# Kernel tuning notes

Hardware: AMD Instinct MI355X
Metric: run time of the kernel (lower is better)

Reference implementation:

```python
import jax, jax.numpy as jnp
import numpy as np
import math

B, N0 = 128, 128          # graphs, nodes per graph
EPG = 512                 # edges per graph
F_IN, EDGE_DIM = 64, 16
EMB, HEADS = 128, 4
HC = EMB * HEADS
L = 2                     # stacked layers (pooling every layer: top_k_every_n=1)
RATIO = 0.5
DENSE = 256


def setup_inputs():
    rng = np.random.default_rng(0)

    def U(fan_in, *shape):
        s = 1.0 / np.sqrt(fan_in)
        return jnp.asarray(rng.uniform(-s, s, shape), dtype=jnp.float32)

    x = jnp.asarray(rng.standard_normal((B * N0, F_IN)), dtype=jnp.float32)
    src = rng.integers(0, N0, (B, EPG))
    dst = rng.integers(0, N0, (B, EPG))
    off = (np.arange(B) * N0)[:, None]
    edge_index = jnp.asarray(np.stack([(src + off).reshape(-1), (dst + off).reshape(-1)]), dtype=jnp.int32)
    edge_attr = jnp.asarray(rng.standard_normal((B * EPG, EDGE_DIM)), dtype=jnp.float32)

    inp = dict(x=x, edge_index=edge_index, edge_attr=edge_attr)
    inp.update(
        c1_Wq=U(F_IN, F_IN, HC), c1_bq=U(F_IN, HC),
        c1_Wk=U(F_IN, F_IN, HC), c1_bk=U(F_IN, HC),
        c1_Wv=U(F_IN, F_IN, HC), c1_bv=U(F_IN, HC),
        c1_We=U(EDGE_DIM, EDGE_DIM, HC),
        c1_Ws=U(F_IN, F_IN, HC), c1_bs=U(F_IN, HC),
        c1_Wb=U(3 * HC, 3 * HC),
        t1_W=U(HC, HC, EMB), t1_b=U(HC, EMB),
        bn1_g=jnp.ones(EMB), bn1_b=jnp.zeros(EMB),
        cl_Wq=U(EMB, L, EMB, HC), cl_bq=U(EMB, L, HC),
        cl_Wk=U(EMB, L, EMB, HC), cl_bk=U(EMB, L, HC),
        cl_Wv=U(EMB, L, EMB, HC), cl_bv=U(EMB, L, HC),
        cl_We=U(EDGE_DIM, L, EDGE_DIM, HC),
        cl_Ws=U(EMB, L, EMB, HC), cl_bs=U(EMB, L, HC),
        cl_Wb=U(3 * HC, L, 3 * HC),
        tl_W=U(HC, L, HC, EMB), tl_b=U(HC, L, EMB),
        bnl_g=jnp.ones((L, EMB)), bnl_b=jnp.zeros((L, EMB)),
        pool_w=U(EMB, L, EMB),
        l1_W=U(2 * EMB, 2 * EMB, DENSE), l1_b=U(2 * EMB, DENSE),
        l2_W=U(DENSE, DENSE, DENSE // 2), l2_b=U(DENSE, DENSE // 2),
        l3_W=U(DENSE // 2, DENSE // 2, 1), l3_b=U(DENSE // 2, 1),
    )
    return inp


def _tconv(x, src, dst, emask, ea, Wq, bq, Wk, bk, Wv, bv, We, Ws, bs, Wb, n_nodes):
    # PyG TransformerConv, beta=True, concat=True, edge features added to key and value
    H, C = HEADS, EMB
    q = (x @ Wq + bq).reshape(-1, H, C)
    k = (x @ Wk + bk).reshape(-1, H, C)
    v = (x @ Wv + bv).reshape(-1, H, C)
    e = (ea @ We).reshape(-1, H, C)
    kj = k[src] + e
    alpha = (q[dst] * kj).sum(-1) * (1.0 / math.sqrt(C))  # [E, H]
    mx = jax.ops.segment_max(jnp.where(emask[:, None], alpha, -jnp.inf), dst, num_segments=n_nodes)
    mx = jnp.where(jnp.isfinite(mx), mx, 0.0)
    p = jnp.where(emask[:, None], jnp.exp(alpha - mx[dst]), 0.0)
    p = p / (jax.ops.segment_sum(p, dst, num_segments=n_nodes)[dst] + 1e-16)
    msg = v[src] + e
    out = jax.ops.segment_sum(p[:, :, None] * msg, dst, num_segments=n_nodes).reshape(-1, H * C)
    skip = x @ Ws + bs
    beta = jax.nn.sigmoid(jnp.concatenate([out, skip, out - skip], -1) @ Wb)[:, None]
    return beta * skip + (1.0 - beta) * out


def _bn(x, g, b):
    # BatchNorm1d, training-mode batch statistics (biased variance)
    m = x.mean(0)
    v = ((x - m) ** 2).mean(0)
    return g * (x - m) * jax.lax.rsqrt(v + 1e-5) + b


def _topk_pool(x, src, dst, emask, w, n):
    # TopKPooling: score = x.w/|w|, keep top ceil(ratio*n) per graph, scale by tanh(score)
    k = int(math.ceil(RATIO * n))
    s = (x @ w) / jnp.linalg.norm(w)          # [B*n]
    _, idx = jax.lax.top_k(s.reshape(B, n), k)
    idx = jnp.sort(idx, axis=1)
    gidx = (jnp.arange(B)[:, None] * n + idx).reshape(-1)
    x_new = x[gidx] * jnp.tanh(s[gidx])[:, None]
    kept = jnp.zeros(B * n, bool).at[gidx].set(True)
    new_id = (jnp.cumsum(kept) - 1).astype(jnp.int32)
    em = emask & kept[src] & kept[dst]
    src_n = jnp.where(em, new_id[src], 0)
    dst_n = jnp.where(em, new_id[dst], 0)
    return x_new, src_n, dst_n, em, k


def _forward(edge_index, x, edge_attr, c1_Wq, c1_bq, c1_Wk, c1_bk, c1_Wv, c1_bv, c1_We, c1_Ws, c1_bs, c1_Wb,
             t1_W, t1_b, bn1_g, bn1_b, cl_Wq, cl_bq, cl_Wk, cl_bk, cl_Wv, cl_bv, cl_We, cl_Ws, cl_bs, cl_Wb,
             tl_W, tl_b, bnl_g, bnl_b, pool_w, l1_W, l1_b, l2_W, l2_b, l3_W, l3_b):
    src, dst = edge_index[0], edge_index[1]
    emask = jnp.ones(src.shape[0], bool)
    n = N0
    x = _tconv(x, src, dst, emask, edge_attr, c1_Wq, c1_bq, c1_Wk, c1_bk, c1_Wv, c1_bv, c1_We, c1_Ws, c1_bs, c1_Wb, B * n)
    x = _bn(jax.nn.relu(x @ t1_W + t1_b), bn1_g, bn1_b)
    reps = []
    for i in range(L):
        x = _tconv(x, src, dst, emask, edge_attr, cl_Wq[i], cl_bq[i], cl_Wk[i], cl_bk[i], cl_Wv[i], cl_bv[i],
                   cl_We[i], cl_Ws[i], cl_bs[i], cl_Wb[i], B * n)
        x = _bn(jax.nn.relu(x @ tl_W[i] + tl_b[i]), bnl_g[i], bnl_b[i])
        x, src, dst, emask, n = _topk_pool(x, src, dst, emask, pool_w[i], n)
        xg = x.reshape(B, n, EMB)
        reps.append(jnp.concatenate([xg.max(1), xg.mean(1)], -1))  # gmp || gap
    h = reps[0]
    for r in reps[1:]:
        h = h + r
    h = jax.nn.relu(h @ l1_W + l1_b)  # dropout p=0.8 is identity at eval
    h = jax.nn.relu(h @ l2_W + l2_b)
    return h @ l3_W + l3_b            # [B, 1]


def reference(x, edge_index, edge_attr, c1_Wq, c1_bq, c1_Wk, c1_bk, c1_Wv, c1_bv, c1_We, c1_Ws, c1_bs, c1_Wb,
              t1_W, t1_b, bn1_g, bn1_b, cl_Wq, cl_bq, cl_Wk, cl_bk, cl_Wv, cl_bv, cl_We, cl_Ws, cl_bs, cl_Wb,
              tl_W, tl_b, bnl_g, bnl_b, pool_w, l1_W, l1_b, l2_W, l2_b, l3_W, l3_b):
    return _forward(edge_index, x, edge_attr, c1_Wq, c1_bq, c1_Wk, c1_bk, c1_Wv, c1_bv, c1_We, c1_Ws, c1_bs, c1_Wb,
                    t1_W, t1_b, bn1_g, bn1_b, cl_Wq, cl_bq, cl_Wk, cl_bk, cl_Wv, cl_bv, cl_We, cl_Ws, cl_bs, cl_Wb,
                    tl_W, tl_b, bnl_g, bnl_b, pool_w, l1_W, l1_b, l2_W, l2_b, l3_W, l3_b)
```

## Files before the change

### kernel.cpp

```cpp
#include <hip/hip_runtime.h>
#include <math.h>

#define E_TOT 65536
#define B_G   128
#define QLD   1664
#define NCOL  1792

typedef __attribute__((ext_vector_type(8))) short short8;
typedef __attribute__((ext_vector_type(4))) short short4v;
typedef __attribute__((ext_vector_type(4))) float float4v;

__device__ __forceinline__ unsigned short f2bf(float f) {
    unsigned int u = __float_as_uint(f);
    unsigned int r = u + 0x7FFFu + ((u >> 16) & 1u);
    return (unsigned short)(r >> 16);
}
__device__ __forceinline__ float bf2f(unsigned short h) {
    return __uint_as_float(((unsigned int)h) << 16);
}

struct LayerPrep {
    const float *Ws, *bs_, *Wq, *bq, *We, *Wv, *bv, *tW;
    float *Wst, *ws_z, *sbt, *zb, *Wu, *bu, *Wet, *wez, *Wvt, *bvt, *Wvz, *bvz;
    unsigned short *Whi, *Wlo;
    int Fin;
};

__device__ __forceinline__ LayerPrep pick(const LayerPrep& p0, const LayerPrep& p1,
                                          const LayerPrep& p2) {
    return blockIdx.y == 0 ? p0 : (blockIdx.y == 1 ? p1 : p2);
}

__global__ void prep_all_k(LayerPrep p0, LayerPrep p1, LayerPrep p2, const float* Wb0,
                           const float* Wb1, const float* Wb2) {
    LayerPrep p = pick(p0, p1, p2);
    const float* Wb = blockIdx.y == 0 ? Wb0 : (blockIdx.y == 1 ? Wb1 : Wb2);
    int Fin = p.Fin;
    int w = blockIdx.x * 4 + (threadIdx.x >> 6);
    int lane = threadIdx.x & 63;

    int U1 = Fin * 2;
    int U2 = U1 + 2;
    int U3 = U2 + Fin * 8;
    int U4 = U3 + 8;
    int U5 = U4 + 128;
    if (w < U5) {
        const float* A; const float* bp; float* outp; int R;
        if (w < U1) {
            int f = w >> 1, m0 = (w & 1) * 64;
            A = p.Ws + (size_t)f * 512; bp = p.tW + m0 + lane;
            outp = p.Wst + f * 128 + m0 + lane; R = 512;
        } else if (w < U2) {
            int m0 = (w - U1) * 64;
            A = p.bs_; bp = p.tW + m0 + lane;
            outp = p.sbt + m0 + lane; R = 512;
        } else if (w < U3) {
            int u = w - U2; int f = u >> 3, q = u & 7;
            int cb = (q >> 1) * 128, m0 = (q & 1) * 64;
            A = p.Wv + (size_t)f * 512 + cb; bp = p.tW + cb * 128 + m0 + lane;
            outp = p.Wvt + (size_t)f * 512 + q * 64 + lane; R = 128;
        } else if (w < U4) {
            int q = w - U3; int cb = (q >> 1) * 128, m0 = (q & 1) * 64;
            A = p.bv + cb; bp = p.tW + cb * 128 + m0 + lane;
            outp = p.bvt + q * 64 + lane; R = 128;
        } else {
            int u = w - U4; int j2 = u >> 1, m0 = (u & 1) * 64;
            int j = j2 & 15, cb = (j2 >> 4) * 128;
            A = p.We + j * 512 + cb; bp = p.tW + cb * 128 + m0 + lane;
            outp = p.Wet + j2 * 128 + m0 + lane; R = 128;
        }
        float a0 = 0.f, a1 = 0.f, a2 = 0.f, a3 = 0.f;
        for (int c = 0; c < R; c += 4) {
            a0 = fmaf(A[c],     bp[0],   a0);
            a1 = fmaf(A[c + 1], bp[128], a1);
            a2 = fmaf(A[c + 2], bp[256], a2);
            a3 = fmaf(A[c + 3], bp[384], a3);
            bp += 512;
        }
        *outp = (a0 + a1) + (a2 + a3);
        return;
    }

    int w2 = w - U5;
    int q1 = Fin, q2 = q1 + 1, q3 = q2 + Fin * 64, q4 = q3 + 64, q5 = q4 + 64;
    int q6 = q5 + Fin * 4, q7 = q6 + 4;
    if (w2 >= q7) return;
    float s = 0.f;
    if (w2 < q1) {
        int f = w2;
        for (int c = lane; c < 512; c += 64)
            s = fmaf(p.Ws[(size_t)f * 512 + c], Wb[512 + c] - Wb[1024 + c], s);
    } else if (w2 < q2) {
        for (int c = lane; c < 512; c += 64)
            s = fmaf(p.bs_[c], Wb[512 + c] - Wb[1024 + c], s);
    } else if (w2 < q3) {
        int q = w2 - q2; int f = q >> 6; int j2 = q & 63;
        int j = j2 & 15; int cb = (j2 >> 4) * 128;
        s = p.Wq[(size_t)f * 512 + cb + lane] * p.We[j * 512 + cb + lane]
          + p.Wq[(size_t)f * 512 + cb + lane + 64] * p.We[j * 512 + cb + lane + 64];
    } else if (w2 < q4) {
        int j2 = w2 - q3; int j = j2 & 15; int cb = (j2 >> 4) * 128;
        s = p.bq[cb + lane] * p.We[j * 512 + cb + lane]
          + p.bq[cb + lane + 64] * p.We[j * 512 + cb + lane + 64];
    } else if (w2 < q5) {
        int j2 = w2 - q4; int j = j2 & 15; int cb = (j2 >> 4) * 128;
        s = p.We[j * 512 + cb + lane] * (Wb[cb + lane] + Wb[1024 + cb + lane])
          + p.We[j * 512 + cb + lane + 64] * (Wb[cb + lane + 64] + Wb[1024 + cb + lane + 64]);
    } else if (w2 < q6) {
        int q = w2 - q5; int f = q >> 2; int cb = (q & 3) * 128;
        s = p.Wv[(size_t)f * 512 + cb + lane] * (Wb[cb + lane] + Wb[1024 + cb + lane])
          + p.Wv[(size_t)f * 512 + cb + lane + 64] * (Wb[cb + lane + 64] + Wb[1024 + cb + lane + 64]);
    } else {
        int cb = (w2 - q6) * 128;
        s = p.bv[cb + lane] * (Wb[cb + lane] + Wb[1024 + cb + lane])
          + p.bv[cb + lane + 64] * (Wb[cb + lane + 64] + Wb[1024 + cb + lane + 64]);
    }
#pragma unroll
    for (int off = 32; off; off >>= 1) s += __shfl_xor(s, off, 64);
    if (lane == 0) {
        if (w2 < q1) p.ws_z[w2] = s;
        else if (w2 < q2) p.zb[0] = s;
        else if (w2 < q3) p.Wu[w2 - q2] = s;
        else if (w2 < q4) p.bu[w2 - q3] = s;
        else if (w2 < q5) p.wez[w2 - q4] = s;
        else if (w2 < q6) p.Wvz[w2 - q5] = s;
        else p.bvz[w2 - q6] = s;
    }
}

__global__ void wsplit_all_k(LayerPrep p0, LayerPrep p1, LayerPrep p2,
                             const float* Wk0, const float* Wk1, const float* Wk2) {
    LayerPrep p = pick(p0, p1, p2);
    const float* Wk = blockIdx.y == 0 ? Wk0 : (blockIdx.y == 1 ? Wk1 : Wk2);
    int K = p.Fin, kshift = (K == 64) ? 6 : 7;
    int idx = blockIdx.x * 256 + threadIdx.x;
    if (idx >= NCOL * K) return;
    int col = idx >> kshift, k = idx & (K - 1);
    float w;
    if (col < 128)       w = p.Wst[k * 128 + col];
    else if (col < 640)  w = p.Wq[(size_t)k * 512 + col - 128];
    else if (col < 1152) w = Wk[(size_t)k * 512 + col - 640];
    else if (col < 1664) w = p.Wvt[(size_t)k * 512 + col - 1152];
    else if (col < 1728) w = p.Wu[(size_t)k * 64 + col - 1664];
    else if (col < 1732) w = p.Wvz[(size_t)k * 4 + col - 1728];
    else if (col == 1732) w = p.ws_z[k];
    else                 w = 0.f;
    unsigned short h = f2bf(w);
    p.Whi[idx] = h;
    p.Wlo[idx] = f2bf(w - bf2f(h));
}

__global__ void xsplit_k(const float* __restrict__ X, int total4,
                         unsigned short* __restrict__ Xhi, unsigned short* __restrict__ Xlo) {
    int idx = blockIdx.x * 256 + threadIdx.x;
    if (idx >= total4) return;
    float4 f = ((const float4*)X)[idx];
    unsigned short h0 = f2bf(f.x), h1 = f2bf(f.y), h2 = f2bf(f.z), h3 = f2bf(f.w);
    short4v hv = {(short)h0, (short)h1, (short)h2, (short)h3};
    short4v lv = {(short)f2bf(f.x - bf2f(h0)), (short)f2bf(f.y - bf2f(h1)),
                  (short)f2bf(f.z - bf2f(h2)), (short)f2bf(f.w - bf2f(h3))};
    *(short4v*)(Xhi + (size_t)idx * 4) = hv;
    *(short4v*)(Xlo + (size_t)idx * 4) = lv;
}

template <int KT>
__global__ __launch_bounds__(256) void qkvs_mfma(
        const unsigned short* __restrict__ Xhi, const unsigned short* __restrict__ Xlo,
        const unsigned short* __restrict__ Whi, const unsigned short* __restrict__ Wlo,
        const float* __restrict__ bq, const float* __restrict__ bk,
        const float* __restrict__ bvt, const float* __restrict__ bu,
        const float* __restrict__ bvz, const float* __restrict__ zb,
        float* __restrict__ out, float* __restrict__ UB, float* __restrict__ VZB,
        float* __restrict__ SZB, int nwg8) {
    constexpr int NKC = KT >> 5;
    constexpr int NCH = KT >> 6;
    __shared__ __align__(16) unsigned short bs[NCH * 2 * 64 * 80];
    const int ldb = 80;
    int tid = threadIdx.x;
    int wave = tid >> 6, lane = tid & 63;
    int m = lane & 15, kg = lane >> 4;
    int hw = blockIdx.y * 28 + blockIdx.x;
    int lb = (hw & 7) * nwg8 + (hw >> 3);
    int rb = (lb / 28) * 256;
    int c0 = (lb % 28) * 64;

    short8 ahi[2][NKC], alo[2][NKC];
    auto loadA = [&](int n0) {
#pragma unroll
        for (int rt = 0; rt < 2; ++rt) {
            const unsigned short* xh = Xhi + (size_t)(n0 + rt * 16 + m) * KT + kg * 8;
            const unsigned short* xl = Xlo + (size_t)(n0 + rt * 16 + m) * KT + kg * 8;
#pragma unroll
            for (int kc = 0; kc < NKC; ++kc) {
                ahi[rt][kc] = *(const short8*)(xh + kc * 32);
                alo[rt][kc] = *(const short8*)(xl + kc * 32);
            }
        }
    };
    loadA(rb + wave * 32);

    for (int i = tid; i < NCH * 64 * 8; i += 256) {
        int ch = i >> 9;
        int r = i & 511; int col = r >> 3, part = r & 7;
        unsigned short* dst = bs + ch * (2 * 64 * 80);
        *(short8*)(dst + col * ldb + part * 8) =
            *(const short8*)(Whi + (size_t)(c0 + col) * KT + ch * 64 + part * 8);
        *(short8*)(dst + 64 * 80 + col * ldb + part * 8) =
            *(const short8*)(Wlo + (size_t)(c0 + col) * KT + ch * 64 + part * 8);
    }
    __syncthreads();

    float bias[4];
#pragma unroll
    for (int ct = 0; ct < 4; ++ct) {
        int col = c0 + ct * 16 + m;
        float bv_;
        if (col < 128)       bv_ = 0.f;
        else if (col < 640)  bv_ = bq[col - 128];
        else if (col < 1152) bv_ = bk[col - 640];
        else if (col < 1664) bv_ = bvt[col - 1152];
        else if (col < 1728) bv_ = bu[col - 1664];
        else if (col < 1732) bv_ = bvz[col - 1728];
        else if (col == 1732) bv_ = zb[0];
        else                 bv_ = 0.f;
        bias[ct] = bv_;
    }

#pragma unroll
    for (int rg = 0; rg < 2; ++rg) {
        int n0 = rb + rg * 128 + wave * 32;
        if (rg) loadA(n0);

        float4v acc[2][4];
#pragma unroll
        for (int rt = 0; rt < 2; ++rt)
#pragma unroll
            for (int ct = 0; ct < 4; ++ct) acc[rt][ct] = (float4v){0.f, 0.f, 0.f, 0.f};

#pragma unroll
        for (int ch = 0; ch < NCH; ++ch) {
            const unsigned short* bsc = bs + ch * (2 * 64 * 80);
#pragma unroll
            for (int kc2 = 0; kc2 < 2; ++kc2) {
                const int kc = ch * 2 + kc2;
#pragma unroll
                for (int ct = 0; ct < 4; ++ct) {
                    const unsigned short* bp = bsc + (ct * 16 + m) * ldb + kg * 8 + kc2 * 32;
                    short8 bhi = *(const short8*)(bp);
                    short8 blo = *(const short8*)(bp + 64 * 80);
                    acc[0][ct] = __builtin_amdgcn_mfma_f32_16x16x32_bf16(ahi[0][kc], bhi, acc[0][ct], 0, 0, 0);
                    acc[0][ct] = __builtin_amdgcn_mfma_f32_16x16x32_bf16(alo[0][kc], bhi, acc[0][ct], 0, 0, 0);
                    acc[0][ct] = __builtin_amdgcn_mfma_f32_16x16x32_bf16(ahi[0][kc], blo, acc[0][ct], 0, 0, 0);
                    acc[1][ct] = __builtin_amdgcn_mfma_f32_16x16x32_bf16(ahi[1][kc], bhi, acc[1][ct], 0, 0, 0);
                    acc[1][ct] = __builtin_amdgcn_mfma_f32_16x16x32_bf16(alo[1][kc], bhi, acc[1][ct], 0, 0, 0);
                    acc[1][ct] = __builtin_amdgcn_mfma_f32_16x16x32_bf16(ahi[1][kc], blo, acc[1][ct], 0, 0, 0);
                }
            }
        }

#pragma unroll
        for (int ct = 0; ct < 4; ++ct) {
            int col = c0 + ct * 16 + m;
            if (col > 1732) continue;
#pragma unroll
            for (int rt = 0; rt < 2; ++rt) {
#pragma unroll
                for (int r = 0; r < 4; ++r) {
                    int row = n0 + rt * 16 + kg * 4 + r;
                    float v = acc[rt][ct][r] + bias[ct];
                    if (col < 1664)      out[(size_t)row * QLD + col] = v;
                    else if (col < 1728) UB[(size_t)row * 64 + col - 1664] = v;
                    else if (col < 1732) VZB[(size_t)row * 4 + col - 1728] = v;
                    else                 SZB[row] = v;
                }
            }
        }
    }
}

__global__ __launch_bounds__(128) void csr_graph_k(const int* __restrict__ src,
                                                   const int* __restrict__ dst,
                                                   int* __restrict__ row_start,
                                                   int* __restrict__ row_end,
                                                   int* __restrict__ colb,
                                                   int* __restrict__ eidb) {
    __shared__ int cnt[128], pref[128], cur[128];
    int g = blockIdx.x, t = threadIdx.x;
    cnt[t] = 0;
    __syncthreads();
    int e0 = g * 512, nb = g * 128;
    int dl[4], sl[4];
#pragma unroll
    for (int i = 0; i < 4; ++i) {
        int e = e0 + t + i * 128;
        dl[i] = dst[e] - nb;
        sl[i] = src[e];
        atomicAdd(&cnt[dl[i]], 1);
    }
    __syncthreads();
    pref[t] = cnt[t];
    __syncthreads();
    for (int st = 1; st < 128; st <<= 1) {
        int v = (t >= st) ? pref[t - st] : 0;
        __syncthreads();
        pref[t] += v;
        __syncthreads();
    }
    int ex = pref[t] - cnt[t];
    row_start[nb + t] = e0 + ex;
    row_end[nb + t]   = e0 + pref[t];
    cur[t] = ex;
    __syncthreads();
#pragma unroll
    for (int i = 0; i < 4; ++i) {
        int pos = atomicAdd(&cur[dl[i]], 1);
        colb[e0 + pos] = sl[i];
        eidb[e0 + pos] = e0 + t + i * 128;
    }
}

__global__ __launch_bounds__(256) void attn_combine_k(
        const float* __restrict__ QB, const float* __restrict__ UB,
        const float* __restrict__ VZB, const float* __restrict__ SZB,
        const int* __restrict__ row_start, const int* __restrict__ row_end,
        const int* __restrict__ colb, const int* __restrict__ eidb,
        const float* __restrict__ ea, const float* __restrict__ wez,
        const float* __restrict__ Wet, const float* __restrict__ sbt,
        const float* __restrict__ tb, float* __restrict__ xn, int nwg8) {
    __shared__ float shO[4][4][128];
    __shared__ float tsh[4][64];
    __shared__ float zsh[4][4];
    int tid = threadIdx.x;
    int head = tid >> 6, lane = tid & 63;
    int grp = lane >> 4, li = lane & 15;
    int bid = blockIdx.x;
    int lb = (bid & 7) * nwg8 + (bid >> 3);
    int node = lb * 4 + grp;

    float wezv = wez[head * 16 + li];
    const float* Qr = QB + (size_t)node * QLD + 128 + head * 128 + li * 8;
    float4 q0 = *(const float4*)Qr;
    float4 q1 = *(const float4*)(Qr + 4);
    float uu = UB[(size_t)node * 64 + head * 16 + li];
    int beg = row_start[node], end = row_end[node];

    float l = 0.f, t = 0.f, zac = 0.f;
    float4 a0 = {0.f, 0.f, 0.f, 0.f}, a1 = {0.f, 0.f, 0.f, 0.f};
    const float scale = 0.08838834764831845f;
    int j = beg;
    for (; j + 1 < end; j += 2) {
        int s1 = colb[j],     e1 = eidb[j];
        int s2 = colb[j + 1], e2 = eidb[j + 1];
        const float* K1 = QB + (size_t)s1 * QLD + 640 + head * 128 + li * 8;
        const float* V1 = QB + (size_t)s1 * QLD + 1152 + head * 128 + li * 8;
        const float* K2 = QB + (size_t)s2 * QLD + 640 + head * 128 + li * 8;
        const float* V2 = QB + (size_t)s2 * QLD + 1152 + head * 128 + li * 8;
        float4 k10 = *(const float4*)K1, k11 = *(const float4*)(K1 + 4);
        float4 v10 = *(const float4*)V1, v11 = *(const float4*)(V1 + 4);
        float4 k20 = *(const float4*)K2, k21 = *(const float4*)(K2 + 4);
        float4 v20 = *(const float4*)V2, v21 = *(const float4*)(V2 + 4);
        float ea1 = ea[(size_t)e1 * 16 + li];
        float ea2 = ea[(size_t)e2 * 16 + li];
        float vz1 = VZB[(size_t)s1 * 4 + head];
        float vz2 = VZB[(size_t)s2 * 4 + head];
        float p1 = q0.x * k10.x + q0.y * k10.y + q0.z * k10.z + q0.w * k10.w
                 + q1.x * k11.x + q1.y * k11.y + q1.z * k11.z + q1.w * k11.w + ea1 * uu;
        float p2 = q0.x * k20.x + q0.y * k20.y + q0.z * k20.z + q0.w * k20.w
                 + q1.x * k21.x + q1.y * k21.y + q1.z * k21.z + q1.w * k21.w + ea2 * uu;
        p1 += __shfl_xor(p1, 1, 64); p1 += __shfl_xor(p1, 2, 64);
        p1 += __shfl_xor(p1, 4, 64); p1 += __shfl_xor(p1, 8, 64);
        p2 += __shfl_xor(p2, 1, 64); p2 += __shfl_xor(p2, 2, 64);
        p2 += __shfl_xor(p2, 4, 64); p2 += __shfl_xor(p2, 8, 64);
        float w1 = expf(p1 * scale), w2 = expf(p2 * scale);
        l += w1; l += w2;
        t = fmaf(w1, ea1, t); t = fmaf(w2, ea2, t);
        zac = fmaf(w1, vz1, zac); zac = fmaf(w2, vz2, zac);
        a0.x = fmaf(w1, v10.x, a0.x); a0.y = fmaf(w1, v10.y, a0.y);
        a0.z = fmaf(w1, v10.z, a0.z); a0.w = fmaf(w1, v10.w, a0.w);
        a1.x = fmaf(w1, v11.x, a1.x); a1.y = fmaf(w1, v11.y, a1.y);
        a1.z = fmaf(w1, v11.z, a1.z); a1.w = fmaf(w1, v11.w, a1.w);
        a0.x = fmaf(w2, v20.x, a0.x); a0.y = fmaf(w2, v20.y, a0.y);
        a0.z = fmaf(w2, v20.z, a0.z); a0.w = fmaf(w2, v20.w, a0.w);
        a1.x = fmaf(w2, v21.x, a1.x); a1.y = fmaf(w2, v21.y, a1.y);
        a1.z = fmaf(w2, v21.z, a1.z); a1.w = fmaf(w2, v21.w, a1.w);
    }
    if (j < end) {
        int s1 = colb[j], e1 = eidb[j];
        const float* K1 = QB + (size_t)s1 * QLD + 640 + head * 128 + li * 8;
        const float* V1 = QB + (size_t)s1 * QLD + 1152 + head * 128 + li * 8;
        float4 k10 = *(const float4*)K1, k11 = *(const float4*)(K1 + 4);
        float4 v10 = *(const float4*)V1, v11 = *(const float4*)(V1 + 4);
        float ea1 = ea[(size_t)e1 * 16 + li];
        float vz1 = VZB[(size_t)s1 * 4 + head];
        float p1 = q0.x * k10.x + q0.y * k10.y + q0.z * k10.z + q0.w * k10.w
                 + q1.x * k11.x + q1.y * k11.y + q1.z * k11.z + q1.w * k11.w + ea1 * uu;
        p1 += __shfl_xor(p1, 1, 64); p1 += __shfl_xor(p1, 2, 64);
        p1 += __shfl_xor(p1, 4, 64); p1 += __shfl_xor(p1, 8, 64);
        float w1 = expf(p1 * scale);
        l += w1;
        t = fmaf(w1, ea1, t);
        zac = fmaf(w1, vz1, zac);
        a0.x = fmaf(w1, v10.x, a0.x); a0.y = fmaf(w1, v10.y, a0.y);
        a0.z = fmaf(w1, v10.z, a0.z); a0.w = fmaf(w1, v10.w, a0.w);
        a1.x = fmaf(w1, v11.x, a1.x); a1.y = fmaf(w1, v11.y, a1.y);
        a1.z = fmaf(w1, v11.z, a1.z); a1.w = fmaf(w1, v11.w, a1.w);
    }

    float inv = 1.f / (l + 1e-16f);
    float tn = t * inv;
    float zw = tn * wezv;
    zw += __shfl_xor(zw, 1, 64); zw += __shfl_xor(zw, 2, 64);
    zw += __shfl_xor(zw, 4, 64); zw += __shfl_xor(zw, 8, 64);
    float z = zac * inv + zw;

    float* op = &shO[grp][head][li * 8];
    op[0] = a0.x * inv; op[1] = a0.y * inv; op[2] = a0.z * inv; op[3] = a0.w * inv;
    op[4] = a1.x * inv; op[5] = a1.y * inv; op[6] = a1.z * inv; op[7] = a1.w * inv;
    tsh[grp][head * 16 + li] = tn;
    if (li == 0) zsh[grp][head] = z;
    __syncthreads();

    int dim = tid & 127;
    int nsBase = tid >> 7;
    float sb = sbt[dim], tbv = tb[dim];
    float wet0 = 0.f, wet1 = 0.f;
#pragma unroll 8
    for (int jj = 0; jj < 64; ++jj) {
        float wv = Wet[jj * 128 + dim];
        wet0 = fmaf(tsh[nsBase][jj], wv, wet0);
        wet1 = fmaf(tsh[nsBase + 2][jj], wv, wet1);
    }
#pragma unroll
    for (int r = 0; r < 2; ++r) {
        int ns = nsBase + r * 2;
        float wet = r ? wet1 : wet0;
        int nd = lb * 4 + ns;
        float outT = shO[ns][0][dim] + shO[ns][1][dim] + shO[ns][2][dim] + shO[ns][3][dim] + wet;
        float zt = zsh[ns][0] + zsh[ns][1] + zsh[ns][2] + zsh[ns][3] + SZB[nd];
        float beta = 1.f / (1.f + expf(-zt));
        float S = QB[(size_t)nd * QLD + dim];
        float a = beta * (S + sb) + (1.f - beta) * outT + tbv;
        xn[(size_t)nd * 128 + dim] = fmaxf(a, 0.f);
    }
}

__global__ void bn_stats_k(const float* __restrict__ x, int N, float* __restrict__ stats) {
    int c = threadIdx.x;
    float s = 0.f, ss = 0.f;
    for (int n = blockIdx.x; n < N; n += gridDim.x) {
        float v = x[(size_t)n * 128 + c];
        s += v; ss += v * v;
    }
    atomicAdd(&stats[c], s);
    atomicAdd(&stats[128 + c], ss);
}

__global__ void bn_apply_k(float* __restrict__ x, int N, const float* __restrict__ stats,
                           const float* __restrict__ g, const float* __restrict__ b,
                           unsigned short* __restrict__ Xhi, unsigned short* __restrict__ Xlo) {
    int idx = blockIdx.x * blockDim.x + threadIdx.x;
    if (idx >= N * 128) return;
    int c = idx & 127;
    float m = stats[c] / (float)N;
    float var = fmaxf(stats[128 + c] / (float)N - m * m, 0.f);
    float inv = rsqrtf(var + 1e-5f);
    float v = g[c] * (x[idx] - m) * inv + b[c];
    x[idx] = v;
    unsigned short h = f2bf(v);
    Xhi[idx] = h;
    Xlo[idx] = f2bf(v - bf2f(h));
}

__global__ void bn_apply_score_k(float* __restrict__ x, int N, const float* __restrict__ stats,
                                 const float* __restrict__ g, const float* __restrict__ b,
                                 const float* __restrict__ w, float* __restrict__ s) {
    int node = blockIdx.x * 4 + (threadIdx.x >> 6);
    int lane = threadIdx.x & 63;
    int c0 = lane, c1 = lane + 64;
    float m0 = stats[c0] / (float)N;
    float v0 = fmaxf(stats[128 + c0] / (float)N - m0 * m0, 0.f);
    float m1 = stats[c1] / (float)N;
    float v1 = fmaxf(stats[128 + c1] / (float)N - m1 * m1, 0.f);
    float* row = x + (size_t)node * 128;
    float x0 = g[c0] * (row[c0] - m0) * rsqrtf(v0 + 1e-5f) + b[c0];
    float x1 = g[c1] * (row[c1] - m1) * rsqrtf(v1 + 1e-5f) + b[c1];
    row[c0] = x0;
    row[c1] = x1;
    float w0 = w[c0], w1 = w[c1];
    float p  = x0 * w0 + x1 * w1;
    float nw = w0 * w0 + w1 * w1;
#pragma unroll
    for (int off = 32; off; off >>= 1) {
        p  += __shfl_xor(p, off, 64);
        nw += __shfl_xor(nw, off, 64);
    }
    if (lane == 0) s[node] = p / sqrtf(nw);
}

__global__ __launch_bounds__(128) void topk_pool0_k(
        const float* __restrict__ sc, const float* __restrict__ x,
        const int* __restrict__ src, const int* __restrict__ dst,
        float* __restrict__ xp, float* __restrict__ rep,
        int* __restrict__ row_start, int* __restrict__ row_end,
        int* __restrict__ colb, int* __restrict__ eidb,
        unsigned short* __restrict__ Xhi, unsigned short* __restrict__ Xlo) {
    __shared__ float ls[128], th[64];
    __shared__ int lk[128], rk[128], oon[64];
    __shared__ int cnt[64], pref[64], cur[64];
    int g = blockIdx.x, t = threadIdx.x;
    float val = sc[g * 128 + t];
    ls[t] = val;
    __syncthreads();
    int c = 0;
    for (int j = 0; j < 128; ++j) {
        float vj = ls[j];
        c += (vj > val || (vj == val && j < t)) ? 1 : 0;
    }
    int kp = (c < 64) ? 1 : 0;
    lk[t] = kp;
    __syncthreads();
    int r = 0;
    for (int j = 0; j < t; ++j) r += lk[j];
    rk[t] = r;
    if (kp) { oon[r] = t; th[r] = tanhf(val); }
    __syncthreads();
    float mx = -INFINITY, sm = 0.f;
    for (int rr = 0; rr < 64; ++rr) {
        float v = x[(size_t)(g * 128 + oon[rr]) * 128 + t] * th[rr];
        int oidx = (g * 64 + rr) * 128 + t;
        xp[oidx] = v;
        unsigned short h = f2bf(v);
        Xhi[oidx] = h;
        Xlo[oidx] = f2bf(v - bf2f(h));
        mx = fmaxf(mx, v);
        sm += v;
    }
    rep[g * 256 + t] = mx;
    rep[g * 256 + 128 + t] = sm * (1.f / 64.f);
    if (t < 64) cnt[t] = 0;
    __syncthreads();
    int e0 = g * 512, nb = g * 128;
    int keepE[4], dr[4], sr[4];
#pragma unroll
    for (int i = 0; i < 4; ++i) {
        int e = e0 + t + i * 128;
        int s_ = src[e] - nb, d_ = dst[e] - nb;
        int ke = lk[s_] && lk[d_];
        keepE[i] = ke;
        dr[i] = rk[d_];
        sr[i] = rk[s_];
        if (ke) atomicAdd(&cnt[dr[i]], 1);
    }
    __syncthreads();
    if (t < 64) pref[t] = cnt[t];
    __syncthreads();
    for (int st = 1; st < 64; st <<= 1) {
        int v = (t < 64 && t >= st) ? pref[t - st] : 0;
        __syncthreads();
        if (t < 64) pref[t] += v;
        __syncthreads();
    }
    if (t < 64) {
        int ex = pref[t] - cnt[t];
        row_start[g * 64 + t] = e0 + ex;
        row_end[g * 64 + t]   = e0 + pref[t];
        cur[t] = ex;
    }
    __syncthreads();
#pragma unroll
    for (int i = 0; i < 4; ++i) {
        if (keepE[i]) {
            int pos = atomicAdd(&cur[dr[i]], 1);
            colb[e0 + pos] = g * 64 + sr[i];
            eidb[e0 + pos] = e0 + t + i * 128;
        }
    }
}

__global__ __launch_bounds__(128) void topk_pool1_k(
        const float* __restrict__ sc, const float* __restrict__ x,
        float* __restrict__ rep) {
    __shared__ float ls[64], th[32];
    __shared__ int lk[64], oon[32];
    int g = blockIdx.x, t = threadIdx.x;
    float val = 0.f;
    if (t < 64) { val = sc[g * 64 + t]; ls[t] = val; }
    __syncthreads();
    if (t < 64) {
        int c = 0;
        for (int j = 0; j < 64; ++j) {
            float vj = ls[j];
            c += (vj > val || (vj == val && j < t)) ? 1 : 0;
        }
        int kp = (c < 32) ? 1 : 0;
        lk[t] = kp;
    }
    __syncthreads();
    if (t < 64 && lk[t]) {
        int r = 0;
        for (int j = 0; j < t; ++j) r += lk[j];
        oon[r] = t;
        th[r] = tanhf(val);
    }
    __syncthreads();
    float mx = -INFINITY, sm = 0.f;
    for (int rr = 0; rr < 32; ++rr) {
        float v = x[(size_t)(g * 64 + oon[rr]) * 128 + t] * th[rr];
        mx = fmaxf(mx, v);
        sm += v;
    }
    rep[g * 256 + t] = mx;
    rep[g * 256 + 128 + t] = sm * (1.f / 32.f);
}

__global__ void head_k(const float* __restrict__ rep0, const float* __restrict__ rep1,
                       const float* __restrict__ W1, const float* __restrict__ b1,
                       const float* __restrict__ W2, const float* __restrict__ b2,
                       const float* __restrict__ W3, const float* __restrict__ b3,
                       float* __restrict__ out) {
    __shared__ float h[256], a1[256], a2[128], red[256];
    int g = blockIdx.x, t = threadIdx.x;
    h[t] = rep0[g * 256 + t] + rep1[g * 256 + t];
    __syncthreads();
    float acc = b1[t];
    for (int i = 0; i < 256; ++i) acc = fmaf(h[i], W1[i * 256 + t], acc);
    a1[t] = fmaxf(acc, 0.f);
    __syncthreads();
    if (t < 128) {
        float a = b2[t];
        for (int i = 0; i < 256; ++i) a = fmaf(a1[i], W2[i * 128 + t], a);
        a2[t] = fmaxf(a, 0.f);
    }
    __syncthreads();
    red[t] = (t < 128) ? a2[t] * W3[t] : 0.f;
    __syncthreads();
    for (int st = 128; st; st >>= 1) {
        if (t < st) red[t] += red[t + st];
        __syncthreads();
    }
    if (t == 0) out[g] = red[0] + b3[0];
}

extern "C" void kernel_launch(void* const* d_in, const int* in_sizes, int n_in,
                              void* d_out, int out_size, void* d_ws, size_t ws_size,
                              hipStream_t stream) {
    (void)in_sizes; (void)n_in; (void)out_size; (void)ws_size;

    const float* x0    = (const float*)d_in[0];
    const int*   ei    = (const int*)d_in[1];
    const float* ea    = (const float*)d_in[2];
    const float* c1_Wq = (const float*)d_in[3];
    const float* c1_bq = (const float*)d_in[4];
    const float* c1_Wk = (const float*)d_in[5];
    const float* c1_bk = (const float*)d_in[6];
    const float* c1_Wv = (const float*)d_in[7];
    const float* c1_bv = (const float*)d_in[8];
    const float* c1_We = (const float*)d_in[9];
    const float* c1_Ws = (const float*)d_in[10];
    const float* c1_bs = (const float*)d_in[11];
    const float* c1_Wb = (const float*)d_in[12];
    const float* t1_W  = (const float*)d_in[13];
    const float* t1_b  = (const float*)d_in[14];
    const float* bn1_g = (const float*)d_in[15];
    const float* bn1_b = (const float*)d_in[16];
    const float* cl_Wq = (const float*)d_in[17];
    const float* cl_bq = (const float*)d_in[18];
    const float* cl_Wk = (const float*)d_in[19];
    const float* cl_bk = (const float*)d_in[20];
    const float* cl_Wv = (const float*)d_in[21];
    const float* cl_bv = (const float*)d_in[22];
    const float* cl_We = (const float*)d_in[23];
    const float* cl_Ws = (const float*)d_in[24];
    const float* cl_bs = (const float*)d_in[25];
    const float* cl_Wb = (const float*)d_in[26];
    const float* tl_W  = (const float*)d_in[27];
    const float* tl_b  = (const float*)d_in[28];
    const float* bnl_g = (const float*)d_in[29];
    const float* bnl_b = (const float*)d_in[30];
    const float* pool_w= (const float*)d_in[31];
    const float* l1_W  = (const float*)d_in[32];
    const float* l1_b  = (const float*)d_in[33];
    const float* l2_W  = (const float*)d_in[34];
    const float* l2_b  = (const float*)d_in[35];
    const float* l3_W  = (const float*)d_in[36];
    const float* l3_b  = (const float*)d_in[37];
    float* out = (float*)d_out;

    char* base = (char*)d_ws;
    size_t off = 0;
    auto alloc = [&](size_t bytes) -> void* {
        void* p = base + off;
        off += (bytes + 255) & ~(size_t)255;
        return p;
    };
    float* QB   = (float*)alloc((size_t)16384 * QLD * 4);
    float* xA   = (float*)alloc((size_t)16384 * 128 * 4);
    float* xB   = (float*)alloc((size_t)16384 * 128 * 4);
    float* UB   = (float*)alloc((size_t)16384 * 64 * 4);
    float* VZB  = (float*)alloc((size_t)16384 * 4 * 4);
    float* SZB  = (float*)alloc((size_t)16384 * 4);
    float* stats  = (float*)alloc(256 * 4);
    float* scores = (float*)alloc(16384 * 4);
    float* rep0   = (float*)alloc(128 * 256 * 4);
    float* rep1   = (float*)alloc(128 * 256 * 4);
    int* row_start = (int*)alloc(16384 * 4);
    int* row_end   = (int*)alloc(16384 * 4);
    int* colb      = (int*)alloc(E_TOT * 4);
    int* eidb      = (int*)alloc(E_TOT * 4);
    unsigned short* Xhi = (unsigned short*)alloc((size_t)16384 * 128 * 2);
    unsigned short* Xlo = (unsigned short*)alloc((size_t)16384 * 128 * 2);

    LayerPrep P[3];
    const float* Wb_[3] = {c1_Wb, cl_Wb, cl_Wb + 1536};
    const float* Wk_[3] = {c1_Wk, cl_Wk, cl_Wk + 65536};
    for (int l = 0; l < 3; ++l) {
        LayerPrep& p = P[l];
        p.Wst  = (float*)alloc(128 * 128 * 4);
        p.ws_z = (float*)alloc(128 * 4);
        p.sbt  = (float*)alloc(128 * 4);
        p.zb   = (float*)alloc(16);
        p.Wu   = (float*)alloc(128 * 64 * 4);
        p.bu   = (float*)alloc(64 * 4);
        p.Wet  = (float*)alloc(64 * 128 * 4);
        p.wez  = (float*)alloc(64 * 4);
        p.Wvt  = (float*)alloc(128 * 512 * 4);
        p.bvt  = (float*)alloc(512 * 4);
        p.Wvz  = (float*)alloc(128 * 4 * 4);
        p.bvz  = (float*)alloc(16);
        p.Whi  = (unsigned short*)alloc((size_t)NCOL * 128 * 2);
        p.Wlo  = (unsigned short*)alloc((size_t)NCOL * 128 * 2);
    }
    P[0].Ws = c1_Ws; P[0].bs_ = c1_bs; P[0].Wq = c1_Wq; P[0].bq = c1_bq;
    P[0].We = c1_We; P[0].Wv = c1_Wv; P[0].bv = c1_bv; P[0].tW = t1_W; P[0].Fin = 64;
    P[1].Ws = cl_Ws; P[1].bs_ = cl_bs; P[1].Wq = cl_Wq; P[1].bq = cl_bq;
    P[1].We = cl_We; P[1].Wv = cl_Wv; P[1].bv = cl_bv; P[1].tW = tl_W; P[1].Fin = 128;
    P[2].Ws = cl_Ws + 65536; P[2].bs_ = cl_bs + 512; P[2].Wq = cl_Wq + 65536;
    P[2].bq = cl_bq + 512; P[2].We = cl_We + 8192; P[2].Wv = cl_Wv + 65536;
    P[2].bv = cl_bv + 512; P[2].tW = tl_W + 65536; P[2].Fin = 128;

    float* xp = xA;

    {
        int unitsMax = (10 * 128 + 138) + (69 * 128 + 133);
        prep_all_k<<<dim3((unitsMax + 3) / 4, 3), 256, 0, stream>>>(P[0], P[1], P[2],
                                                                    Wb_[0], Wb_[1], Wb_[2]);
        wsplit_all_k<<<dim3((NCOL * 128 + 255) / 256, 3), 256, 0, stream>>>(P[0], P[1], P[2],
                                                                            Wk_[0], Wk_[1], Wk_[2]);
    }

    csr_graph_k<<<B_G, 128, 0, stream>>>(ei, ei + E_TOT, row_start, row_end, colb, eidb);
    xsplit_k<<<(16384 * 64 / 4 + 255) / 256, 256, 0, stream>>>(x0, 16384 * 64 / 4, Xhi, Xlo);

    auto tconv = [&](int L, int N, const float* bq, const float* bk, const float* tb,
                     float* xn) {
        int nwg8 = 28 * (N / 256) / 8;
        if (P[L].Fin == 64)
            qkvs_mfma<64><<<dim3(28, N / 256), 256, 0, stream>>>(Xhi, Xlo, P[L].Whi, P[L].Wlo,
                                                                 bq, bk, P[L].bvt, P[L].bu,
                                                                 P[L].bvz, P[L].zb,
                                                                 QB, UB, VZB, SZB, nwg8);
        else
            qkvs_mfma<128><<<dim3(28, N / 256), 256, 0, stream>>>(Xhi, Xlo, P[L].Whi, P[L].Wlo,
                                                                  bq, bk, P[L].bvt, P[L].bu,
                                                                  P[L].bvz, P[L].zb,
                                                                  QB, UB, VZB, SZB, nwg8);
        attn_combine_k<<<N / 4, 256, 0, stream>>>(QB, UB, VZB, SZB,
                                                  row_start, row_end, colb, eidb,
                                                  ea, P[L].wez, P[L].Wet, P[L].sbt, tb,
                                                  xn, N / 32);
    };

    tconv(0, 16384, c1_bq, c1_bk, t1_b, xA);
    hipMemsetAsync(stats, 0, 256 * 4, stream);
    bn_stats_k<<<512, 128, 0, stream>>>(xA, 16384, stats);
    bn_apply_k<<<(16384 * 128 + 255) / 256, 256, 0, stream>>>(xA, 16384, stats, bn1_g, bn1_b,
                                                              Xhi, Xlo);

    tconv(1, 16384, cl_bq, cl_bk, tl_b, xB);
    hipMemsetAsync(stats, 0, 256 * 4, stream);
    bn_stats_k<<<512, 128, 0, stream>>>(xB, 16384, stats);
    bn_apply_score_k<<<16384 / 4, 256, 0, stream>>>(xB, 16384, stats, bnl_g, bnl_b,
                                                    pool_w, scores);

    topk_pool0_k<<<B_G, 128, 0, stream>>>(scores, xB, ei, ei + E_TOT, xp, rep0,
                                          row_start, row_end, colb, eidb, Xhi, Xlo);

    tconv(2, 8192, cl_bq + 512, cl_bk + 512, tl_b + 128, xB);
    hipMemsetAsync(stats, 0, 256 * 4, stream);
    bn_stats_k<<<512, 128, 0, stream>>>(xB, 8192, stats);
    bn_apply_score_k<<<8192 / 4, 256, 0, stream>>>(xB, 8192, stats, bnl_g + 128, bnl_b + 128,
                                                   pool_w + 128, scores);

    topk_pool1_k<<<B_G, 128, 0, stream>>>(scores, xB, rep1);

    head_k<<<B_G, 256, 0, stream>>>(rep0, rep1, l1_W, l1_b, l2_W, l2_b, l3_W, l3_b, out);
}
```

Measured before the change: 521.8 us.

## Halve qkvs GEMM row tile and stream weight chunks through register double-buffer

The QKV/skip GEMM kernel now handles 128 rows per workgroup instead of 256, which doubles the grid and removes the second row-group pass. Weight tiles are no longer staged into LDS all at once. Each 64-wide K chunk is prefetched into registers one step ahead and written into a single-chunk LDS buffer, which cuts LDS use and overlaps global loads with MFMA work. The cost is that weight tiles are loaded from global memory twice as often across the grid, and there is an extra barrier per chunk.

```diff
diff --git a/kernel.cpp b/kernel.cpp
--- a/kernel.cpp
+++ b/kernel.cpp
@@ -174,105 +174,102 @@
         float* __restrict__ SZB, int nwg8) {
     constexpr int NKC = KT >> 5;
     constexpr int NCH = KT >> 6;
-    __shared__ __align__(16) unsigned short bs[NCH * 2 * 64 * 80];
-    const int ldb = 80;
+    __shared__ __align__(16) unsigned short bs[2 * 64 * 80];
+    const int ldb = 80, loHalf = 64 * 80;
     int tid = threadIdx.x;
     int wave = tid >> 6, lane = tid & 63;
     int m = lane & 15, kg = lane >> 4;
     int hw = blockIdx.y * 28 + blockIdx.x;
     int lb = (hw & 7) * nwg8 + (hw >> 3);
-    int rb = (lb / 28) * 256;
+    int n0 = (lb / 28) * 128 + wave * 32;
     int c0 = (lb % 28) * 64;
 
     short8 ahi[2][NKC], alo[2][NKC];
-    auto loadA = [&](int n0) {
-#pragma unroll
-        for (int rt = 0; rt < 2; ++rt) {
-            const unsigned short* xh = Xhi + (size_t)(n0 + rt * 16 + m) * KT + kg * 8;
-            const unsigned short* xl = Xlo + (size_t)(n0 + rt * 16 + m) * KT + kg * 8;
-#pragma unroll
-            for (int kc = 0; kc < NKC; ++kc) {
-                ahi[rt][kc] = *(const short8*)(xh + kc * 32);
-                alo[rt][kc] = *(const short8*)(xl + kc * 32);
+#pragma unroll
+    for (int rt = 0; rt < 2; ++rt) {
+        const unsigned short* xh = Xhi + (size_t)(n0 + rt * 16 + m) * KT + kg * 8;
+        const unsigned short* xl = Xlo + (size_t)(n0 + rt * 16 + m) * KT + kg * 8;
+#pragma unroll
+        for (int kc = 0; kc < NKC; ++kc) {
+            ahi[rt][kc] = *(const short8*)(xh + kc * 32);
+            alo[rt][kc] = *(const short8*)(xl + kc * 32);
+        }
+    }
+
+    float4v acc[2][4];
+#pragma unroll
+    for (int rt = 0; rt < 2; ++rt)
+#pragma unroll
+        for (int ct = 0; ct < 4; ++ct) acc[rt][ct] = (float4v){0.f, 0.f, 0.f, 0.f};
+
+    short8 ph[2][2], pl[2][2];
+#pragma unroll
+    for (int it = 0; it < 2; ++it) {
+        int i = tid + it * 256; int col = i >> 3, part = i & 7;
+        ph[0][it] = *(const short8*)(Whi + (size_t)(c0 + col) * KT + part * 8);
+        pl[0][it] = *(const short8*)(Wlo + (size_t)(c0 + col) * KT + part * 8);
+    }
+
+#pragma unroll
+    for (int ch = 0; ch < NCH; ++ch) {
+        if (ch) __syncthreads();
+#pragma unroll
+        for (int it = 0; it < 2; ++it) {
+            int i = tid + it * 256; int col = i >> 3, part = i & 7;
+            *(short8*)(bs + col * ldb + part * 8) = ph[ch & 1][it];
+            *(short8*)(bs + loHalf + col * ldb + part * 8) = pl[ch & 1][it];
+        }
+        __syncthreads();
+        if (ch + 1 < NCH) {
+#pragma unroll
+            for (int it = 0; it < 2; ++it) {
+                int i = tid + it * 256; int col = i >> 3, part = i & 7;
+                ph[(ch + 1) & 1][it] =
+                    *(const short8*)(Whi + (size_t)(c0 + col) * KT + (ch + 1) * 64 + part * 8);
+                pl[(ch + 1) & 1][it] =
+                    *(const short8*)(Wlo + (size_t)(c0 + col) * KT + (ch + 1) * 64 + part * 8);
             }
         }
-    };
-    loadA(rb + wave * 32);
-
-    for (int i = tid; i < NCH * 64 * 8; i += 256) {
-        int ch = i >> 9;
-        int r = i & 511; int col = r >> 3, part = r & 7;
-        unsigned short* dst = bs + ch * (2 * 64 * 80);
-        *(short8*)(dst + col * ldb + part * 8) =
-            *(const short8*)(Whi + (size_t)(c0 + col) * KT + ch * 64 + part * 8);
-        *(short8*)(dst + 64 * 80 + col * ldb + part * 8) =
-            *(const short8*)(Wlo + (size_t)(c0 + col) * KT + ch * 64 + part * 8);
-    }
-    __syncthreads();
-
-    float bias[4];
+#pragma unroll
+        for (int kc2 = 0; kc2 < 2; ++kc2) {
+            const int kc = ch * 2 + kc2;
+#pragma unroll
+            for (int ct = 0; ct < 4; ++ct) {
+                const unsigned short* bp = bs + (ct * 16 + m) * ldb + kg * 8 + kc2 * 32;
+                short8 bhi = *(const short8*)(bp);
+                short8 blo = *(const short8*)(bp + loHalf);
+                acc[0][ct] = __builtin_amdgcn_mfma_f32_16x16x32_bf16(ahi[0][kc], bhi, acc[0][ct], 0, 0, 0);
+                acc[0][ct] = __builtin_amdgcn_mfma_f32_16x16x32_bf16(alo[0][kc], bhi, acc[0][ct], 0, 0, 0);
+                acc[0][ct] = __builtin_amdgcn_mfma_f32_16x16x32_bf16(ahi[0][kc], blo, acc[0][ct], 0, 0, 0);
+                acc[1][ct] = __builtin_amdgcn_mfma_f32_16x16x32_bf16(ahi[1][kc], bhi, acc[1][ct], 0, 0, 0);
+                acc[1][ct] = __builtin_amdgcn_mfma_f32_16x16x32_bf16(alo[1][kc], bhi, acc[1][ct], 0, 0, 0);
+                acc[1][ct] = __builtin_amdgcn_mfma_f32_16x16x32_bf16(ahi[1][kc], blo, acc[1][ct], 0, 0, 0);
+            }
+        }
+    }
+
 #pragma unroll
     for (int ct = 0; ct < 4; ++ct) {
         int col = c0 + ct * 16 + m;
-        float bv_;
-        if (col < 128)       bv_ = 0.f;
-        else if (col < 640)  bv_ = bq[col - 128];
-        else if (col < 1152) bv_ = bk[col - 640];
-        else if (col < 1664) bv_ = bvt[col - 1152];
-        else if (col < 1728) bv_ = bu[col - 1664];
-        else if (col < 1732) bv_ = bvz[col - 1728];
-        else if (col == 1732) bv_ = zb[0];
-        else                 bv_ = 0.f;
-        bias[ct] = bv_;
-    }
-
-#pragma unroll
-    for (int rg = 0; rg < 2; ++rg) {
-        int n0 = rb + rg * 128 + wave * 32;
-        if (rg) loadA(n0);
-
-        float4v acc[2][4];
-#pragma unroll
-        for (int rt = 0; rt < 2; ++rt)
-#pragma unroll
-            for (int ct = 0; ct < 4; ++ct) acc[rt][ct] = (float4v){0.f, 0.f, 0.f, 0.f};
-
-#pragma unroll
-        for (int ch = 0; ch < NCH; ++ch) {
-            const unsigned short* bsc = bs + ch * (2 * 64 * 80);
-#pragma unroll
-            for (int kc2 = 0; kc2 < 2; ++kc2) {
-                const int kc = ch * 2 + kc2;
-#pragma unroll
-                for (int ct = 0; ct < 4; ++ct) {
-                    const unsigned short* bp = bsc + (ct * 16 + m) * ldb + kg * 8 + kc2 * 32;
-                    short8 bhi = *(const short8*)(bp);
-                    short8 blo = *(const short8*)(bp + 64 * 80);
-                    acc[0][ct] = __builtin_amdgcn_mfma_f32_16x16x32_bf16(ahi[0][kc], bhi, acc[0][ct], 0, 0, 0);
-                    acc[0][ct] = __builtin_amdgcn_mfma_f32_16x16x32_bf16(alo[0][kc], bhi, acc[0][ct], 0, 0, 0);
-                    acc[0][ct] = __builtin_amdgcn_mfma_f32_16x16x32_bf16(ahi[0][kc], blo, acc[0][ct], 0, 0, 0);
-                    acc[1][ct] = __builtin_amdgcn_mfma_f32_16x16x32_bf16(ahi[1][kc], bhi, acc[1][ct], 0, 0, 0);
-                    acc[1][ct] = __builtin_amdgcn_mfma_f32_16x16x32_bf16(alo[1][kc], bhi, acc[1][ct], 0, 0, 0);
-                    acc[1][ct] = __builtin_amdgcn_mfma_f32_16x16x32_bf16(ahi[1][kc], blo, acc[1][ct], 0, 0, 0);
-                }
-            }
-        }
-
-#pragma unroll
-        for (int ct = 0; ct < 4; ++ct) {
-            int col = c0 + ct * 16 + m;
-            if (col > 1732) continue;
-#pragma unroll
-            for (int rt = 0; rt < 2; ++rt) {
-#pragma unroll
-                for (int r = 0; r < 4; ++r) {
-                    int row = n0 + rt * 16 + kg * 4 + r;
-                    float v = acc[rt][ct][r] + bias[ct];
-                    if (col < 1664)      out[(size_t)row * QLD + col] = v;
-                    else if (col < 1728) UB[(size_t)row * 64 + col - 1664] = v;
-                    else if (col < 1732) VZB[(size_t)row * 4 + col - 1728] = v;
-                    else                 SZB[row] = v;
-                }
+        if (col > 1732) continue;
+        float bias;
+        if (col < 128)       bias = 0.f;
+        else if (col < 640)  bias = bq[col - 128];
+        else if (col < 1152) bias = bk[col - 640];
+        else if (col < 1664) bias = bvt[col - 1152];
+        else if (col < 1728) bias = bu[col - 1664];
+        else if (col < 1732) bias = bvz[col - 1728];
+        else                 bias = zb[0];
+#pragma unroll
+        for (int rt = 0; rt < 2; ++rt) {
+#pragma unroll
+            for (int r = 0; r < 4; ++r) {
+                int row = n0 + rt * 16 + kg * 4 + r;
+                float v = acc[rt][ct][r] + bias;
+                if (col < 1664)      out[(size_t)row * QLD + col] = v;
+                else if (col < 1728) UB[(size_t)row * 64 + col - 1664] = v;
+                else if (col < 1732) VZB[(size_t)row * 4 + col - 1728] = v;
+                else                 SZB[row] = v;
             }
         }
     }
@@ -753,14 +750,14 @@
 
     auto tconv = [&](int L, int N, const float* bq, const float* bk, const float* tb,
                      float* xn) {
-        int nwg8 = 28 * (N / 256) / 8;
+        int nwg8 = 28 * (N / 128) / 8;
         if (P[L].Fin == 64)
-            qkvs_mfma<64><<<dim3(28, N / 256), 256, 0, stream>>>(Xhi, Xlo, P[L].Whi, P[L].Wlo,
+            qkvs_mfma<64><<<dim3(28, N / 128), 256, 0, stream>>>(Xhi, Xlo, P[L].Whi, P[L].Wlo,
                                                                  bq, bk, P[L].bvt, P[L].bu,
                                                                  P[L].bvz, P[L].zb,
                                                                  QB, UB, VZB, SZB, nwg8);
         else
-            qkvs_mfma<128><<<dim3(28, N / 256), 256, 0, stream>>>(Xhi, Xlo, P[L].Whi, P[L].Wlo,
+            qkvs_mfma<128><<<dim3(28, N / 128), 256, 0, stream>>>(Xhi, Xlo, P[L].Whi, P[L].Wlo,
                                                                   bq, bk, P[L].bvt, P[L].bu,
                                                                   P[L].bvz, P[L].zb,
                                                                   QB, UB, VZB, SZB, nwg8);
```

After: 502.9 us. 3.6% less time.
